# Performance work log

Measured on AMD Instinct MI355X. Metric: run time of the kernel, lower is better.

The kernel has to match this reference:

```python
import jax, jax.numpy as jnp
import numpy as np
import math

R, S, HC, MAX_L = 4, 6, 64, 100
NH = R + 2 * S  # 16 heads
D = NH * HC     # 1024


def _signed_pow(base, L):
    # base: [h,1,1] (possibly negative), L: [t,t] integer-valued float
    mag = jnp.exp(L * jnp.log(jnp.abs(base)))
    sgn = jnp.where(base < 0, 1.0 - 2.0 * (L % 2), 1.0)
    return mag * sgn


def setup_inputs() -> dict:
    key = jax.random.key(0)
    ks = jax.random.split(key, 12)
    b, t = 4, 2048
    x = jax.random.normal(ks[0], (b, t, D), dtype=jnp.float32)
    mu = jax.random.uniform(ks[1], (1,), minval=-3.0, maxval=3.0)
    flag = jnp.where(jax.random.randint(ks[2], (R,), 0, 2) == 0, -1.0, 1.0)
    lam = (jax.random.uniform(ks[3], (R,), minval=0.6, maxval=0.98) * flag)[:, None, None]
    gamma_c1 = jnp.tanh(jax.random.uniform(ks[4], (S,)) + 1.0)[:, None, None]
    gamma_c2 = jnp.tanh(jax.random.uniform(ks[5], (S,)) + 1.0)[:, None, None]
    theta_c1 = jnp.full((S, 1, 1), math.pi / 4, dtype=jnp.float32)
    theta_c2 = jnp.full((S, 1, 1), math.pi / 4, dtype=jnp.float32)
    sc = 1.0 / np.sqrt(D)
    Wq = jax.random.normal(ks[6], (D, D), dtype=jnp.float32) * sc
    Wk = jax.random.normal(ks[7], (D, D), dtype=jnp.float32) * sc
    Wv = jax.random.normal(ks[8], (D, D), dtype=jnp.float32) * sc
    Wf = jax.random.normal(ks[9], (D, D), dtype=jnp.float32) * sc
    bq = jnp.zeros((D,)); bk = jnp.zeros((D,)); bv = jnp.zeros((D,)); bf = jnp.zeros((D,))
    return dict(x=x, mu=mu, lam=lam, gamma_c1=gamma_c1, gamma_c2=gamma_c2,
                theta_c1=theta_c1, theta_c2=theta_c2,
                Wq=Wq, bq=bq, Wk=Wk, bk=bk, Wv=Wv, bv=bv, Wf=Wf, bf=bf)


def _positional(t, lam, gamma_c1, gamma_c2, theta_c1, theta_c2, dtype):
    # L[i,j] = min(max(i-j,0), MAX_L); strictly-lower-triangular mask
    mask = jnp.tril(jnp.ones((t, t), dtype=dtype), -1)
    L = jnp.minimum(jnp.cumsum(mask, axis=0), float(MAX_L))
    P_R = _signed_pow(lam, L) * mask                                   # [r,t,t]
    P_C1 = _signed_pow(gamma_c1, L) * mask * jnp.sin(theta_c1 * L)     # [s,t,t]
    P_C2 = _signed_pow(gamma_c2, L) * mask * jnp.cos(theta_c2 * L)     # [s,t,t]
    return jnp.concatenate([P_R, P_C1, P_C2], axis=0)                  # [H,t,t]


def reference(x, mu, lam, gamma_c1, gamma_c2, theta_c1, theta_c2,
              Wq, bq, Wk, bk, Wv, bv, Wf, bf):
    b, t, d = x.shape
    P = _positional(t, lam, gamma_c1, gamma_c2, theta_c1, theta_c2, x.dtype)
    Q = (x @ Wq.T + bq).reshape(b, t, NH, HC)
    K = (x @ Wk.T + bk).reshape(b, t, NH, HC)
    V = (x @ Wv.T + bv).reshape(b, t, NH, HC)
    scores = jnp.einsum('bqhd,bkhd->bhqk', Q, K)  # no 1/sqrt(d) scaling (faithful)
    att = jax.nn.softmax(scores, axis=-1)
    w = jax.nn.sigmoid(mu)[0]
    blend = (1.0 - w) * att + w * P[None]         # [b,H,t,t]
    out = jnp.einsum('bhqk,bkhd->bqhd', blend, V).reshape(b, t, NH * HC)
    return out @ Wf.T + bf
```

## Files before the change

kernel.cpp:

```cpp
#include <hip/hip_runtime.h>
#include <math.h>
#include <stdint.h>
#include <stddef.h>

typedef _Float16 f16;
typedef _Float16 f16x8 __attribute__((ext_vector_type(8)));
typedef _Float16 f16x4 __attribute__((ext_vector_type(4)));
typedef __fp16 fp16x2 __attribute__((ext_vector_type(2)));
typedef float f32x4 __attribute__((ext_vector_type(4)));
typedef float f32x16 __attribute__((ext_vector_type(16)));
typedef float fvec4 __attribute__((ext_vector_type(4)));
typedef unsigned int u32x4 __attribute__((ext_vector_type(4)));
typedef int i32x2 __attribute__((ext_vector_type(2)));

#define MFMA16F16(a, b, c) __builtin_amdgcn_mfma_f32_16x16x32_f16((a), (b), (c), 0, 0, 0)
#define MFMA32F16(a, b, c) __builtin_amdgcn_mfma_f32_32x32x16_f16((a), (b), (c), 0, 0, 0)

static constexpr int kT = 2048;
static constexpr int kB = 4;
static constexpr int kD = 1024;
static constexpr int kNH = 16;
static constexpr int kM = kB * kT;
static constexpr int kMAXL = 100;
static constexpr float kLOG2E = 1.4426950408889634f;

static constexpr size_t SZ_XH = (size_t)kM * kD * 2;
static constexpr size_t SZ_W = (size_t)kD * kD * 2;
static constexpr size_t OFF_TAB = 0;
static constexpr size_t OFF_XH = 8192;
static constexpr size_t OFF_WQ = OFF_XH + SZ_XH;
static constexpr size_t OFF_WK = OFF_WQ + SZ_W;
static constexpr size_t OFF_WV = OFF_WK + SZ_W;
static constexpr size_t OFF_WF = OFF_WV + SZ_W;
static constexpr size_t OFF_Q = OFF_WF + SZ_W;
static constexpr size_t OFF_K = OFF_Q + SZ_XH;
static constexpr size_t OFF_V = OFF_K + SZ_XH;
static constexpr size_t OFF_P = OFF_V + SZ_XH;
static constexpr size_t WS_NEED = OFF_P + SZ_XH;

__device__ __forceinline__ unsigned int pk_f16(float a, float b) {
  fp16x2 h = __builtin_amdgcn_cvt_pkrtz(a, b);
  return __builtin_bit_cast(unsigned int, h);
}

__device__ __forceinline__ i32x2 pl32swap(unsigned a, unsigned b) {
  return __builtin_amdgcn_permlane32_swap((int)a, (int)b, false, false);
}

__global__ void pre_kernel(const float* __restrict__ x, const float* __restrict__ Wq,
                           const float* __restrict__ Wk, const float* __restrict__ Wv,
                           const float* __restrict__ Wf, const float* __restrict__ mu,
                           const float* __restrict__ lam, const float* __restrict__ g1,
                           const float* __restrict__ g2, const float* __restrict__ th1,
                           const float* __restrict__ th2, f16* __restrict__ xh,
                           f16* __restrict__ wqh, f16* __restrict__ wkh, f16* __restrict__ wvh,
                           f16* __restrict__ wfh, float* __restrict__ tab) {
  const int b = blockIdx.x;
  if (b == 0) {
    const float w = 1.0f / (1.0f + expf(-mu[0]));
    for (int e = threadIdx.x; e < kNH * (kMAXL + 1); e += blockDim.x) {
      const int h = e / (kMAXL + 1);
      const int L = e - h * (kMAXL + 1);
      const float Lf = (float)L;
      float v;
      if (h < 4) {
        const float base = lam[h];
        const float mag = expf(Lf * logf(fabsf(base)));
        const float sgn = (base < 0.0f && (L & 1)) ? -1.0f : 1.0f;
        v = mag * sgn;
      } else if (h < 10) {
        const int s = h - 4;
        v = expf(Lf * logf(g1[s])) * sinf(th1[s] * Lf);
      } else {
        const int s = h - 10;
        v = expf(Lf * logf(g2[s])) * cosf(th2[s] * Lf);
      }
      tab[e] = w * v;
    }
    if (threadIdx.x == 0) tab[kNH * (kMAXL + 1)] = 1.0f - w;
  }

  const float* src;
  f16* dst;
  int n4, i0, nb;
  if (b < 2048) {
    src = x; dst = xh; n4 = kM * kD / 4; i0 = b; nb = 2048;
  } else {
    const int wsel = (b - 2048) >> 8;
    const int wb = (b - 2048) & 255;
    src = (wsel == 0) ? Wq : ((wsel == 1) ? Wk : ((wsel == 2) ? Wv : Wf));
    dst = (wsel == 0) ? wqh : ((wsel == 1) ? wkh : ((wsel == 2) ? wvh : wfh));
    n4 = kD * kD / 4; i0 = wb; nb = 256;
  }
  for (int i = i0 * 256 + threadIdx.x; i < n4; i += nb * 256) {
    fvec4 v = ((const fvec4*)src)[i];
    f16x4 o;
    o[0] = (f16)v[0]; o[1] = (f16)v[1]; o[2] = (f16)v[2]; o[3] = (f16)v[3];
    ((f16x4*)dst)[i] = o;
  }
}

template <typename OutT, bool BIAS_ROW>
__global__ __launch_bounds__(256, 3) void gemm_bt_kernel(
    const f16* __restrict__ A, const f16* __restrict__ B, const float* __restrict__ bias,
    OutT* __restrict__ C, int M, int N, int K, float oscale) {
  __shared__ f16 As[128][32];
  __shared__ f16 Bs[128][32];
  const int tid = threadIdx.x;
  const int lane = tid & 63;
  const int wave = tid >> 6;
  const int quad = lane >> 4;
  const int l16 = lane & 15;
  const int nb = N >> 7;
  const int bm = blockIdx.x / nb;
  const int bn = blockIdx.x - bm * nb;
  const int m0 = bm << 7;
  const int n0 = bn << 7;
  const int wm = (wave & 1) << 6;
  const int wn = (wave >> 1) << 6;

  const int srow = tid >> 2;
  const int scol = (tid & 3) << 3;
  const f16* Ap = A + (size_t)(m0 + srow) * K + scol;
  const f16* Bp = B + (size_t)(n0 + srow) * K + scol;
  const size_t rstep = (size_t)64 * K;

  f32x4 acc[4][4];
#pragma unroll
  for (int i = 0; i < 4; i++)
#pragma unroll
    for (int j = 0; j < 4; j++) acc[i][j] = (f32x4){0.f, 0.f, 0.f, 0.f};

  f16x8 ra0 = *(const f16x8*)(Ap);
  f16x8 ra1 = *(const f16x8*)(Ap + rstep);
  f16x8 rb0 = *(const f16x8*)(Bp);
  f16x8 rb1 = *(const f16x8*)(Bp + rstep);

  for (int k0 = 0; k0 < K; k0 += 32) {
    __syncthreads();
    *(f16x8*)&As[srow][scol] = ra0;
    *(f16x8*)&As[srow + 64][scol] = ra1;
    *(f16x8*)&Bs[srow][scol] = rb0;
    *(f16x8*)&Bs[srow + 64][scol] = rb1;
    __syncthreads();
    if (k0 + 32 < K) {
      ra0 = *(const f16x8*)(Ap + (k0 + 32));
      ra1 = *(const f16x8*)(Ap + rstep + (k0 + 32));
      rb0 = *(const f16x8*)(Bp + (k0 + 32));
      rb1 = *(const f16x8*)(Bp + rstep + (k0 + 32));
    }
    f16x8 af[4], bf[4];
#pragma unroll
    for (int i = 0; i < 4; i++) af[i] = *(const f16x8*)&As[wm + i * 16 + l16][quad * 8];
#pragma unroll
    for (int i = 0; i < 4; i++) bf[i] = *(const f16x8*)&Bs[wn + i * 16 + l16][quad * 8];
#pragma unroll
    for (int mi = 0; mi < 4; mi++)
#pragma unroll
      for (int ni = 0; ni < 4; ni++) acc[mi][ni] = MFMA16F16(af[mi], bf[ni], acc[mi][ni]);
  }

#pragma unroll
  for (int mi = 0; mi < 4; mi++) {
    const int rbase = m0 + wm + mi * 16 + quad * 4;
#pragma unroll
    for (int ni = 0; ni < 4; ni++) {
      const int gc = n0 + wn + ni * 16 + l16;
      const float bcol = BIAS_ROW ? 0.0f : bias[gc];
#pragma unroll
      for (int r = 0; r < 4; r++) {
        const int gr = rbase + r;
        float v = acc[mi][ni][r] + (BIAS_ROW ? bias[gr] : bcol);
        v *= oscale;
        C[(size_t)gr * N + gc] = (OutT)v;
      }
    }
  }
}

__global__ __launch_bounds__(256, 3) void qkv_kernel(
    const f16* __restrict__ xh, const f16* __restrict__ wq, const f16* __restrict__ wk,
    const f16* __restrict__ wv, const float* __restrict__ bq, const float* __restrict__ bk,
    const float* __restrict__ bv, f16* __restrict__ Qp, f16* __restrict__ Kp,
    f16* __restrict__ Vt) {
  __shared__ f16 As[128][32];
  __shared__ f16 Bs[128][32];
  const int g = blockIdx.x >> 9;
  const int inner = blockIdx.x & 511;
  const f16* A = (g == 2) ? wv : xh;
  const f16* B = (g == 0) ? wq : ((g == 1) ? wk : xh);
  const float* bias = (g == 0) ? bq : ((g == 1) ? bk : bv);
  f16* C = (g == 0) ? Qp : ((g == 1) ? Kp : Vt);
  const int N = (g == 2) ? kM : kD;
  const int K = kD;
  const float oscale = (g == 0) ? kLOG2E : 1.0f;
  const bool bias_row = (g == 2);
  const int nbs = (g == 2) ? 6 : 3;

  const int tid = threadIdx.x;
  const int lane = tid & 63;
  const int wave = tid >> 6;
  const int quad = lane >> 4;
  const int l16 = lane & 15;
  const int bm = inner >> nbs;
  const int bn = inner & ((1 << nbs) - 1);
  const int m0 = bm << 7;
  const int n0 = bn << 7;
  const int wm = (wave & 1) << 6;
  const int wn = (wave >> 1) << 6;

  const int srow = tid >> 2;
  const int scol = (tid & 3) << 3;
  const f16* Ap = A + (size_t)(m0 + srow) * K + scol;
  const f16* Bp = B + (size_t)(n0 + srow) * K + scol;
  const size_t rstep = (size_t)64 * K;

  f32x4 acc[4][4];
#pragma unroll
  for (int i = 0; i < 4; i++)
#pragma unroll
    for (int j = 0; j < 4; j++) acc[i][j] = (f32x4){0.f, 0.f, 0.f, 0.f};

  f16x8 ra0 = *(const f16x8*)(Ap);
  f16x8 ra1 = *(const f16x8*)(Ap + rstep);
  f16x8 rb0 = *(const f16x8*)(Bp);
  f16x8 rb1 = *(const f16x8*)(Bp + rstep);

  for (int k0 = 0; k0 < K; k0 += 32) {
    __syncthreads();
    *(f16x8*)&As[srow][scol] = ra0;
    *(f16x8*)&As[srow + 64][scol] = ra1;
    *(f16x8*)&Bs[srow][scol] = rb0;
    *(f16x8*)&Bs[srow + 64][scol] = rb1;
    __syncthreads();
    if (k0 + 32 < K) {
      ra0 = *(const f16x8*)(Ap + (k0 + 32));
      ra1 = *(const f16x8*)(Ap + rstep + (k0 + 32));
      rb0 = *(const f16x8*)(Bp + (k0 + 32));
      rb1 = *(const f16x8*)(Bp + rstep + (k0 + 32));
    }
    f16x8 af[4], bf[4];
#pragma unroll
    for (int i = 0; i < 4; i++) af[i] = *(const f16x8*)&As[wm + i * 16 + l16][quad * 8];
#pragma unroll
    for (int i = 0; i < 4; i++) bf[i] = *(const f16x8*)&Bs[wn + i * 16 + l16][quad * 8];
#pragma unroll
    for (int mi = 0; mi < 4; mi++)
#pragma unroll
      for (int ni = 0; ni < 4; ni++) acc[mi][ni] = MFMA16F16(af[mi], bf[ni], acc[mi][ni]);
  }

#pragma unroll
  for (int mi = 0; mi < 4; mi++) {
    const int rbase = m0 + wm + mi * 16 + quad * 4;
#pragma unroll
    for (int ni = 0; ni < 4; ni++) {
      const int gc = n0 + wn + ni * 16 + l16;
      const float bcol = bias_row ? 0.0f : bias[gc];
#pragma unroll
      for (int r = 0; r < 4; r++) {
        const int gr = rbase + r;
        float v = acc[mi][ni][r] + (bias_row ? bias[gr] : bcol);
        v *= oscale;
        C[(size_t)gr * N + gc] = (f16)v;
      }
    }
  }
}

__global__ __launch_bounds__(256, 3) void attn_kernel(
    const f16* __restrict__ Qh, const f16* __restrict__ Kh, const f16* __restrict__ Vt,
    const float* __restrict__ tabg, f16* __restrict__ Pb) {
  __shared__ f16 Ks[128][68];
  __shared__ f16 Vs[64][132];
  __shared__ float tab_s[101];

  const int tid = threadIdx.x;
  const int lane = tid & 63;
  const int wave = tid >> 6;
  const int l31 = lane & 31;
  const int hi = lane >> 5;
  const int hi8 = hi * 8;
  const int xcd = blockIdx.x & 7;
  const int rest = blockIdx.x >> 3;
  const int qt = rest & 15;
  const int combo = (rest >> 4) * 8 + xcd;
  const int h = combo & 15;
  const int bi = combo >> 4;

  if (tid < 101) tab_s[tid] = tabg[h * 101 + tid];
  const float one_m_w = tabg[kNH * 101];
  const float tab100f = tabg[h * 101 + kMAXL];

  const int qblk = qt * 128;
  const int qw0 = qblk + wave * 32;
  const int qg = qw0 + l31;
  const size_t bt0 = (size_t)bi * kT;

  f16x8 qf[4];
#pragma unroll
  for (int kc = 0; kc < 4; kc++)
    qf[kc] = *(const f16x8*)(Qh + (bt0 + qg) * kD + h * 64 + kc * 16 + hi8);

  f32x16 Oat[2], Opc[2];
  f32x16 Lacc;
#pragma unroll
  for (int dt = 0; dt < 2; dt++)
#pragma unroll
    for (int r = 0; r < 16; r++) {
      Oat[dt][r] = 0.f;
      Opc[dt][r] = 0.f;
    }
#pragma unroll
  for (int r = 0; r < 16; r++) Lacc[r] = 0.f;
  float mrow = -INFINITY;

  const int sr8 = tid >> 3, sp8 = tid & 7;
  const int sr16 = tid >> 4, sp16 = tid & 15;

  f16x8 cf, ones;
  {
    const f16 cth = (f16)tab100f;
#pragma unroll
    for (int ii = 0; ii < 8; ii++) {
      cf[ii] = cth;
      ones[ii] = (f16)1.0f;
    }
  }

  for (int j0 = 0; j0 < kT; j0 += 128) {
    __syncthreads();
#pragma unroll
    for (int u = 0; u < 4; u++) {
      const int jr = sr8 + u * 32;
      *(f16x8*)&Ks[jr][sp8 * 8] = *(const f16x8*)(Kh + (bt0 + j0 + jr) * kD + h * 64 + sp8 * 8);
    }
#pragma unroll
    for (int u = 0; u < 4; u++) {
      const int d = sr16 + u * 16;
      *(f16x8*)&Vs[d][sp16 * 8] =
          *(const f16x8*)(Vt + (size_t)(h * 64 + d) * kM + bt0 + j0 + sp16 * 8);
    }
    __syncthreads();

#pragma unroll
    for (int c = 0; c < 2; c++) {
      f32x16 s[2];
#pragma unroll
      for (int jt = 0; jt < 2; jt++)
#pragma unroll
        for (int r = 0; r < 16; r++) s[jt][r] = 0.f;
#pragma unroll
      for (int kc = 0; kc < 4; kc++) {
        f16x8 ka = *(const f16x8*)&Ks[c * 64 + l31][kc * 16 + hi8];
        f16x8 kb = *(const f16x8*)&Ks[c * 64 + 32 + l31][kc * 16 + hi8];
        s[0] = MFMA32F16(ka, qf[kc], s[0]);
        s[1] = MFMA32F16(kb, qf[kc], s[1]);
      }

      float mx = s[0][0];
#pragma unroll
      for (int jt = 0; jt < 2; jt++)
#pragma unroll
        for (int r = 0; r < 16; r++) mx = fmaxf(mx, s[jt][r]);
      mx = fmaxf(mx, __shfl_xor(mx, 32));
      if (!__all(mx <= mrow + 8.0f)) {
        const float mnew = fmaxf(mrow, mx);
        const float al = __builtin_amdgcn_exp2f(mrow - mnew);
        mrow = mnew;
#pragma unroll
        for (int dt = 0; dt < 2; dt++)
#pragma unroll
          for (int r = 0; r < 16; r++) Oat[dt][r] *= al;
        Lacc[0] *= al;
      }

#pragma unroll
      for (int jt = 0; jt < 2; jt++) {
        unsigned w[8];
#pragma unroll
        for (int k = 0; k < 8; k++) {
          const float e0 = __builtin_amdgcn_exp2f(s[jt][2 * k] - mrow);
          const float e1 = __builtin_amdgcn_exp2f(s[jt][2 * k + 1] - mrow);
          w[k] = pk_f16(e0, e1);
        }
        i32x2 a0 = pl32swap(w[0], w[2]);
        i32x2 a1 = pl32swap(w[1], w[3]);
        i32x2 b0 = pl32swap(w[4], w[6]);
        i32x2 b1 = pl32swap(w[5], w[7]);
        u32x4 ue = {(unsigned)a0.x, (unsigned)a1.x, (unsigned)a0.y, (unsigned)a1.y};
        u32x4 uo = {(unsigned)b0.x, (unsigned)b1.x, (unsigned)b0.y, (unsigned)b1.y};
        const f16x8 fe = __builtin_bit_cast(f16x8, ue);
        const f16x8 fo = __builtin_bit_cast(f16x8, uo);
#pragma unroll
        for (int dt = 0; dt < 2; dt++) {
          f16x8 ve = *(const f16x8*)&Vs[dt * 32 + l31][c * 64 + jt * 32 + hi8];
          Oat[dt] = MFMA32F16(ve, fe, Oat[dt]);
        }
        Lacc = MFMA32F16(ones, fe, Lacc);
#pragma unroll
        for (int dt = 0; dt < 2; dt++) {
          f16x8 vo = *(const f16x8*)&Vs[dt * 32 + l31][c * 64 + jt * 32 + 16 + hi8];
          Oat[dt] = MFMA32F16(vo, fo, Oat[dt]);
        }
        Lacc = MFMA32F16(ones, fo, Lacc);
      }
    }

    if (j0 + 228 <= qw0) {
#pragma unroll
      for (int jc = 0; jc < 8; jc++)
#pragma unroll
        for (int dt = 0; dt < 2; dt++) {
          f16x8 vf = *(const f16x8*)&Vs[dt * 32 + l31][jc * 16 + hi8];
          Opc[dt] = MFMA32F16(vf, cf, Opc[dt]);
        }
    }
  }

  {
    const float inv = one_m_w / Lacc[0];
#pragma unroll
    for (int dt = 0; dt < 2; dt++)
#pragma unroll
      for (int r = 0; r < 16; r++) Oat[dt][r] = Oat[dt][r] * inv + Opc[dt][r];
  }

#pragma unroll
  for (int tb = 0; tb < 2; tb++) {
    const int jb = qblk - 128 + tb * 128;
    if (jb >= 0) {
      __syncthreads();
#pragma unroll
      for (int u = 0; u < 4; u++) {
        const int d = sr16 + u * 16;
        *(f16x8*)&Vs[d][sp16 * 8] =
            *(const f16x8*)(Vt + (size_t)(h * 64 + d) * kM + bt0 + jb + sp16 * 8);
      }
      __syncthreads();
#pragma unroll
      for (int jc = 0; jc < 8; jc++) {
        f16x8 wf;
#pragma unroll
        for (int e = 0; e < 8; e++) {
          const int j = jb + jc * 16 + hi8 + e;
          const int dlt = qg - j;
          float pv = 0.0f;
          if (dlt > 0) pv = tab_s[dlt > kMAXL ? kMAXL : dlt];
          wf[e] = (f16)pv;
        }
#pragma unroll
        for (int dt = 0; dt < 2; dt++) {
          f16x8 vf = *(const f16x8*)&Vs[dt * 32 + l31][jc * 16 + hi8];
          Oat[dt] = MFMA32F16(vf, wf, Oat[dt]);
        }
      }
    }
  }

  {
    f16* sw = &Ks[wave * 32][0];
#pragma unroll
    for (int dt = 0; dt < 2; dt++)
#pragma unroll
      for (int r = 0; r < 16; r++) {
        const int d = dt * 32 + (r & 3) + 8 * (r >> 2) + 4 * hi;
        sw[l31 * 68 + d] = (f16)Oat[dt][r];
      }
#pragma unroll
    for (int u = 0; u < 4; u++) {
      const int qr = lane >> 1;
      const int c0 = (lane & 1) * 32 + u * 8;
      f16x8 ofr = *(const f16x8*)&sw[qr * 68 + c0];
      *(f16x8*)(Pb + (bt0 + qw0 + qr) * kD + h * 64 + c0) = ofr;
    }
  }
}

extern "C" void kernel_launch(void* const* d_in, const int* in_sizes, int n_in, void* d_out,
                              int out_size, void* d_ws, size_t ws_size, hipStream_t stream) {
  const float* x = (const float*)d_in[0];
  const float* mu = (const float*)d_in[1];
  const float* lam = (const float*)d_in[2];
  const float* g1 = (const float*)d_in[3];
  const float* g2 = (const float*)d_in[4];
  const float* th1 = (const float*)d_in[5];
  const float* th2 = (const float*)d_in[6];
  const float* Wq = (const float*)d_in[7];
  const float* bq = (const float*)d_in[8];
  const float* Wk = (const float*)d_in[9];
  const float* bk = (const float*)d_in[10];
  const float* Wv = (const float*)d_in[11];
  const float* bv = (const float*)d_in[12];
  const float* Wf = (const float*)d_in[13];
  const float* bf = (const float*)d_in[14];

  if (ws_size < WS_NEED) return;

  char* ws = (char*)d_ws;
  float* tab = (float*)(ws + OFF_TAB);
  f16* xh = (f16*)(ws + OFF_XH);
  f16* wqh = (f16*)(ws + OFF_WQ);
  f16* wkh = (f16*)(ws + OFF_WK);
  f16* wvh = (f16*)(ws + OFF_WV);
  f16* wfh = (f16*)(ws + OFF_WF);
  f16* Qp = (f16*)(ws + OFF_Q);
  f16* Kp = (f16*)(ws + OFF_K);
  f16* Vtp = (f16*)(ws + OFF_V);
  f16* Pbp = (f16*)(ws + OFF_P);

  pre_kernel<<<3072, 256, 0, stream>>>(x, Wq, Wk, Wv, Wf, mu, lam, g1, g2, th1, th2, xh, wqh,
                                       wkh, wvh, wfh, tab);

  qkv_kernel<<<1536, 256, 0, stream>>>(xh, wqh, wkh, wvh, bq, bk, bv, Qp, Kp, Vtp);

  attn_kernel<<<1024, 256, 0, stream>>>(Qp, Kp, Vtp, tab, Pbp);

  gemm_bt_kernel<float, false><<<512, 256, 0, stream>>>(Pbp, wfh, bf, (float*)d_out, kM, kD, kD,
                                                        1.0f);
}
```

Baseline: 354.9 us.

## Replace constant-positional MFMA accumulation with precomputed V prefix sums

For key tiles far from the diagonal the positional weight is a constant, so its contribution equals that constant times a sum of V rows. Until now attention recomputed this sum with extra MFMAs on every such tile. A new small kernel computes per-(batch, head) block prefix sums of V once and stores them in the now-unused fp16 x workspace. Attention then adds tab100 times the matching prefix vector in its epilogue. This removes MFMA work and accumulator registers from the main loop, at the cost of an extra launch that reads all of V with only 64 blocks.

New measurement: 346.3 us. -2.4%, faster.

```diff
diff --git a/kernel.cpp b/kernel.cpp
--- a/kernel.cpp
+++ b/kernel.cpp
@@ -37,6 +37,7 @@
 static constexpr size_t OFF_V = OFF_K + SZ_XH;
 static constexpr size_t OFF_P = OFF_V + SZ_XH;
 static constexpr size_t WS_NEED = OFF_P + SZ_XH;
+static constexpr size_t OFF_VPRE = OFF_XH;
 
 __device__ __forceinline__ unsigned int pk_f16(float a, float b) {
   fp16x2 h = __builtin_amdgcn_cvt_pkrtz(a, b);
@@ -100,6 +101,34 @@
   }
 }
 
+__global__ __launch_bounds__(1024) void vsum_kernel(const f16* __restrict__ Vt,
+                                                    float* __restrict__ Vpre) {
+  const int combo = blockIdx.x;
+  const int h = combo & 15;
+  const int bi = combo >> 4;
+  const int d = threadIdx.x >> 4;
+  const int p = threadIdx.x & 15;
+  const f16* src = Vt + (size_t)(h * 64 + d) * kM + (size_t)bi * kT + p * 128;
+  float s = 0.f;
+#pragma unroll
+  for (int j = 0; j < 128; j += 8) {
+    f16x8 v = *(const f16x8*)(src + j);
+#pragma unroll
+    for (int e = 0; e < 8; e++) s += (float)v[e];
+  }
+  __shared__ float ts[64][17];
+  ts[d][p] = s;
+  __syncthreads();
+  if (p == 0) {
+    float acc = 0.f;
+    float* out = Vpre + (size_t)combo * 16 * 64 + d;
+    for (int q = 0; q < 16; q++) {
+      out[q * 64] = acc;
+      acc += ts[d][q];
+    }
+  }
+}
+
 template <typename OutT, bool BIAS_ROW>
 __global__ __launch_bounds__(256, 3) void gemm_bt_kernel(
     const f16* __restrict__ A, const f16* __restrict__ B, const float* __restrict__ bias,
@@ -270,7 +299,7 @@
 
 __global__ __launch_bounds__(256, 3) void attn_kernel(
     const f16* __restrict__ Qh, const f16* __restrict__ Kh, const f16* __restrict__ Vt,
-    const float* __restrict__ tabg, f16* __restrict__ Pb) {
+    const float* __restrict__ tabg, const float* __restrict__ Vpre, f16* __restrict__ Pb) {
   __shared__ f16 Ks[128][68];
   __shared__ f16 Vs[64][132];
   __shared__ float tab_s[101];
@@ -302,15 +331,12 @@
   for (int kc = 0; kc < 4; kc++)
     qf[kc] = *(const f16x8*)(Qh + (bt0 + qg) * kD + h * 64 + kc * 16 + hi8);
 
-  f32x16 Oat[2], Opc[2];
+  f32x16 Oat[2];
   f32x16 Lacc;
 #pragma unroll
   for (int dt = 0; dt < 2; dt++)
 #pragma unroll
-    for (int r = 0; r < 16; r++) {
-      Oat[dt][r] = 0.f;
-      Opc[dt][r] = 0.f;
-    }
+    for (int r = 0; r < 16; r++) Oat[dt][r] = 0.f;
 #pragma unroll
   for (int r = 0; r < 16; r++) Lacc[r] = 0.f;
   float mrow = -INFINITY;
@@ -318,15 +344,9 @@
   const int sr8 = tid >> 3, sp8 = tid & 7;
   const int sr16 = tid >> 4, sp16 = tid & 15;
 
-  f16x8 cf, ones;
-  {
-    const f16 cth = (f16)tab100f;
-#pragma unroll
-    for (int ii = 0; ii < 8; ii++) {
-      cf[ii] = cth;
-      ones[ii] = (f16)1.0f;
-    }
-  }
+  f16x8 ones;
+#pragma unroll
+  for (int ii = 0; ii < 8; ii++) ones[ii] = (f16)1.0f;
 
   for (int j0 = 0; j0 < kT; j0 += 128) {
     __syncthreads();
@@ -406,24 +426,19 @@
         Lacc = MFMA32F16(ones, fo, Lacc);
       }
     }
-
-    if (j0 + 228 <= qw0) {
-#pragma unroll
-      for (int jc = 0; jc < 8; jc++)
-#pragma unroll
-        for (int dt = 0; dt < 2; dt++) {
-          f16x8 vf = *(const f16x8*)&Vs[dt * 32 + l31][jc * 16 + hi8];
-          Opc[dt] = MFMA32F16(vf, cf, Opc[dt]);
-        }
-    }
   }
 
   {
     const float inv = one_m_w / Lacc[0];
+    const int pidx = (qt >= 1) ? (qt - 1) : 0;
+    const float* vp = Vpre + ((size_t)(bi * 16 + h) * 16 + pidx) * 64;
 #pragma unroll
     for (int dt = 0; dt < 2; dt++)
 #pragma unroll
-      for (int r = 0; r < 16; r++) Oat[dt][r] = Oat[dt][r] * inv + Opc[dt][r];
+      for (int r = 0; r < 16; r++) {
+        const int dd = dt * 32 + (r & 3) + 8 * (r >> 2) + 4 * hi;
+        Oat[dt][r] = Oat[dt][r] * inv + tab100f * vp[dd];
+      }
   }
 
 #pragma unroll
@@ -508,13 +523,16 @@
   f16* Kp = (f16*)(ws + OFF_K);
   f16* Vtp = (f16*)(ws + OFF_V);
   f16* Pbp = (f16*)(ws + OFF_P);
+  float* Vpre = (float*)(ws + OFF_VPRE);
 
   pre_kernel<<<3072, 256, 0, stream>>>(x, Wq, Wk, Wv, Wf, mu, lam, g1, g2, th1, th2, xh, wqh,
                                        wkh, wvh, wfh, tab);
 
   qkv_kernel<<<1536, 256, 0, stream>>>(xh, wqh, wkh, wvh, bq, bk, bv, Qp, Kp, Vtp);
 
-  attn_kernel<<<1024, 256, 0, stream>>>(Qp, Kp, Vtp, tab, Pbp);
+  vsum_kernel<<<64, 1024, 0, stream>>>(Vtp, Vpre);
+
+  attn_kernel<<<1024, 256, 0, stream>>>(Qp, Kp, Vtp, tab, Vpre, Pbp);
 
   gemm_bt_kernel<float, false><<<512, 256, 0, stream>>>(Pbp, wfh, bf, (float*)d_out, kM, kD, kD,
                                                         1.0f);
```
